# Optimization experiments

Measured on AMD Instinct MI355X. Metric: run time of the kernel, lower is better.

The kernel has to match this reference:

```python
import jax, jax.numpy as jnp
import numpy as np
from jax import lax

B, DIM, H, W = 32, 256, 64, 64
DS = DIM // 4          # dim_split = 64
MLP_H = int(DIM * 2.0)  # mlp_ratio = 2.0
AK = 11                 # att_kernel
EPS = 1e-5


def conv(x, w, b=None, padding=(0, 0), dilation=1, groups=1, stride=1):
    y = lax.conv_general_dilated(
        x, w, (stride, stride),
        [(padding[0], padding[0]), (padding[1], padding[1])],
        rhs_dilation=(dilation, dilation),
        dimension_numbers=('NCHW', 'OIHW', 'NCHW'),
        feature_group_count=groups)
    if b is not None:
        y = y + b[None, :, None, None]
    return y


def bn(x):
    # BatchNorm2d, training-mode batch stats, affine at default init (gamma=1, beta=0)
    m = x.mean(axis=(0, 2, 3), keepdims=True)
    v = ((x - m) ** 2).mean(axis=(0, 2, 3), keepdims=True)
    return (x - m) * lax.rsqrt(v + EPS)


def maxpool2x2(x):
    b, c, h, w = x.shape
    xw = x.reshape(b, c, h // 2, 2, w // 2, 2).transpose(0, 1, 2, 4, 3, 5).reshape(b, c, h // 2, w // 2, 4)
    return xw.max(axis=-1), jnp.argmax(xw, axis=-1)


def maxunpool2x2(y, idx):
    b, c, h, w = y.shape
    oh = jax.nn.one_hot(idx, 4, dtype=y.dtype)  # scatter back into 2x2 window argmax slot
    out = (y[..., None] * oh).reshape(b, c, h, w, 2, 2).transpose(0, 1, 2, 4, 3, 5)
    return out.reshape(b, c, 2 * h, 2 * w)


def maxpool3(x):
    return lax.reduce_window(x, -jnp.inf, lax.max, (1, 1, 3, 3), (1, 1, 1, 1),
                             [(0, 0), (0, 0), (1, 1), (1, 1)])


def blurpool(x):
    # antialiased_cnns.BlurPool(C, stride=3): filt_size=4, reflect pad (1,2)
    f = jnp.array([1., 3., 3., 1.], dtype=x.dtype)
    k = f[:, None] * f[None, :]
    k = k / k.sum()
    c = x.shape[1]
    wgt = jnp.broadcast_to(k[None, None], (c, 1, 4, 4))
    xp = jnp.pad(x, ((0, 0), (0, 0), (1, 2), (1, 2)), mode='reflect')
    return lax.conv_general_dilated(xp, wgt, (3, 3), [(0, 0), (0, 0)],
                                    dimension_numbers=('NCHW', 'OIHW', 'NCHW'),
                                    feature_group_count=c)


def h_tf(x):
    b, c, hh, ww = x.shape
    x = jnp.pad(x, ((0, 0), (0, 0), (0, 0), (0, ww)))
    x = x.reshape(b, c, -1)[..., :-ww]
    return x.reshape(b, c, hh, 2 * ww - 1)


def inv_h_tf(x):
    b, c, hh, _ = x.shape
    x = x.reshape(b, c, -1)
    x = jnp.pad(x, ((0, 0), (0, 0), (0, hh)))
    return x.reshape(b, c, hh, 2 * hh)[..., :hh]


def v_tf(x):
    return h_tf(x.transpose(0, 1, 3, 2)).transpose(0, 1, 3, 2)


def inv_v_tf(x):
    return inv_h_tf(x.transpose(0, 1, 3, 2)).transpose(0, 1, 3, 2)


def ga12(x, p1w, p1b, c0w, c0b, spw, spb, c1w, c1b, c2w, c2b, cw, cb, sqw, sqb, p2w, p2b):
    xp, idx = maxpool2x2(x)
    c = xp.shape[1]
    h = jax.nn.relu(conv(xp, p1w, p1b))
    a1 = conv(h, c0w, c0b, padding=(2, 2), groups=c)                 # depthwise 5x5
    a2 = conv(a1, spw, spb, padding=(9, 9), dilation=3, groups=c)    # depthwise 7x7 dil3
    a1s = conv(a1, c1w, c1b)
    a2s = conv(a2, c2w, c2b)
    comb = jnp.concatenate([a1s, a2s], axis=1)
    agg = jnp.concatenate([comb.mean(axis=1, keepdims=True),
                           comb.max(axis=1, keepdims=True)], axis=1)
    sig = jax.nn.sigmoid(conv(agg, sqw, sqb, padding=(3, 3)))
    attn = conv(a1s * sig[:, 0:1] + a2s * sig[:, 1:2], cw, cb)
    h = conv(h * attn, p2w, p2b)
    return maxunpool2x2(h, idx)


def setup_inputs() -> dict:
    key = jax.random.key(0)
    ks = jax.random.split(key, 32)
    r = lambda i, shape: jax.random.normal(ks[i], shape, jnp.float32) * 0.05
    return {
        'x': jax.random.normal(ks[0], (B, DIM, H, W), jnp.float32),
        'pa_w1': r(1, (4 * DS, DS, 1, 1)),
        'pa_w2': r(2, (DS, 4 * DS, 1, 1)),
        'la_w': r(3, (DS, DS, 3, 3)),
        'mra_h1': r(4, (DS, 1, AK, 3)),
        'mra_v1': r(5, (DS, 1, 3, AK)),
        'mra_h2': r(6, (DS, 1, AK, 3)),
        'mra_v2': r(7, (DS, 1, 3, AK)),
        'g_proj1_w': r(8, (DS, DS, 1, 1)), 'g_proj1_b': r(9, (DS,)),
        'g_conv0_w': r(10, (DS, 1, 5, 5)), 'g_conv0_b': r(11, (DS,)),
        'g_sp_w': r(12, (DS, 1, 7, 7)), 'g_sp_b': r(13, (DS,)),
        'g_c1_w': r(14, (DS // 2, DS, 1, 1)), 'g_c1_b': r(15, (DS // 2,)),
        'g_c2_w': r(16, (DS // 2, DS, 1, 1)), 'g_c2_b': r(17, (DS // 2,)),
        'g_c_w': r(18, (DS, DS // 2, 1, 1)), 'g_c_b': r(19, (DS,)),
        'g_sq_w': r(20, (2, 2, 7, 7)), 'g_sq_b': r(21, (2,)),
        'g_proj2_w': r(22, (DS, DS, 1, 1)), 'g_proj2_b': r(23, (DS,)),
        'mlp_w1': r(24, (MLP_H, DIM, 1, 1)),
        'mlp_w2': r(25, (DIM, MLP_H, 1, 1)),
    }


def reference(x, pa_w1, pa_w2, la_w, mra_h1, mra_v1, mra_h2, mra_v2,
              g_proj1_w, g_proj1_b, g_conv0_w, g_conv0_b, g_sp_w, g_sp_b,
              g_c1_w, g_c1_b, g_c2_w, g_c2_b, g_c_w, g_c_b,
              g_sq_w, g_sq_b, g_proj2_w, g_proj2_b, mlp_w1, mlp_w2):
    x1, x2, x3, x4 = jnp.split(x, 4, axis=1)
    # PA: pixel attention (1x1 expand -> BN -> ReLU -> 1x1) sigmoid gate
    xa1 = x1 * jax.nn.sigmoid(conv(jax.nn.relu(bn(conv(x1, pa_w1))), pa_w2))
    # LA: 3x3 conv -> BN -> ReLU
    xa2 = jax.nn.relu(bn(conv(x2, la_w, padding=(1, 1))))
    # MRA: maxpool3x3 -> blurpool(stride3) -> 4 strip depthwise convs (+diag shear) -> BN -> sigmoid -> nearest upsample gate
    xm = blurpool(maxpool3(x3))
    ph, pv = (AK // 2, 1), (1, AK // 2)
    xh1 = conv(xm, mra_h1, padding=ph, groups=DS)
    xw1 = conv(xm, mra_v1, padding=pv, groups=DS)
    xh2 = inv_h_tf(conv(h_tf(xm), mra_h2, padding=ph, groups=DS))
    xw2 = inv_v_tf(conv(v_tf(xm), mra_v2, padding=pv, groups=DS))
    gate = jax.nn.sigmoid(bn(xh1 + xw1 + xh2 + xw2))
    hs, ws = gate.shape[-2:]
    ri = (jnp.arange(H) * hs) // H   # torch F.interpolate mode='nearest' index rule
    ci = (jnp.arange(W) * ws) // W
    xa3 = x3 * gate[:, :, ri][:, :, :, ci]
    # D_GA (stage==2): maxpool -> GA12 -> BN -> maxunpool
    x4p, idx1 = maxpool2x2(x4)
    xg = ga12(x4p, g_proj1_w, g_proj1_b, g_conv0_w, g_conv0_b, g_sp_w, g_sp_b,
              g_c1_w, g_c1_b, g_c2_w, g_c2_b, g_c_w, g_c_b, g_sq_w, g_sq_b,
              g_proj2_w, g_proj2_b)
    xa4 = maxunpool2x2(bn(xg), idx1)
    x_att = jnp.concatenate([xa1, xa2, xa3, xa4], axis=1)
    # residual MLP (drop_path=0 -> identity)
    return x + conv(jax.nn.relu(bn(conv(x_att, mlp_w1))), mlp_w2)
```

## Files before the change

### kernel.cpp

```cpp
#include <hip/hip_runtime.h>
#include <hip/hip_bf16.h>
#include <math.h>

typedef __hip_bfloat16 bf16;
typedef __attribute__((ext_vector_type(4))) float f32x4;
typedef __attribute__((ext_vector_type(8))) short s16x8;
typedef __attribute__((ext_vector_type(4))) short s16x4;

static __device__ __forceinline__ float bits2f(short s){ return __uint_as_float(((unsigned)(unsigned short)s)<<16); }
static __device__ __forceinline__ short bfbits(float f){ bf16 h = __float2bfloat16(f); return *reinterpret_cast<short*>(&h); }
static __device__ __forceinline__ float ldf(float v){ return v; }
static __device__ __forceinline__ float sigm(float v){ return 1.f/(1.f+__expf(-v)); }

#define P_IMG 4096

#define GLDS16(SRC, DST) __builtin_amdgcn_global_load_lds( \
    (__attribute__((address_space(1))) void*)(SRC), \
    (__attribute__((address_space(3))) void*)(DST), 16, 0, 0)

namespace {
constexpr long long XATT_OFF = 0;
constexpr long long BIG_OFF  = 67108864;
constexpr long long MISC     = 134217728;
constexpr long long XM_OFF   = MISC;
constexpr long long MSUM_OFF = MISC + 3964928;
constexpr long long SH_OFF   = MISC + 7929856;
constexpr long long SH2_OFF  = MISC + 15679488;
constexpr long long X4P_OFF  = MISC + 23429120;
constexpr long long IDX1_OFF = MISC + 31817728;
constexpr long long XP_OFF   = MISC + 40206336;
constexpr long long IDX2_OFF = MISC + 42303488;
constexpr long long HBUF_OFF = MISC + 44400640;
constexpr long long A1_OFF   = MISC + 46497792;
constexpr long long A2_OFF   = MISC + 48594944;
constexpr long long A1S_OFF  = MISC + 50692096;
constexpr long long A2S_OFF  = MISC + 51740672;
constexpr long long AGG_OFF  = MISC + 52789248;
constexpr long long SIG_OFF  = MISC + 52854784;
constexpr long long ATTN_OFF = MISC + 52920320;
constexpr long long H2_OFF   = MISC + 55017472;
constexpr long long XG_OFF   = MISC + 57114624;
constexpr long long P33_OFF  = 201326592;
constexpr long long STATS_OFF= 234881024;
constexpr long long WS_NEED  = 234897408;
constexpr long long XPM_OFF  = MISC;
constexpr long long YLA_OFF  = MISC + 33554432;
}

__global__ __launch_bounds__(256) void zero_out_k(float* __restrict__ o, int n){
    int i = blockIdx.x*256 + threadIdx.x;
    if (i < n) o[i] = 0.f;
}

__global__ __launch_bounds__(256) void packw_k(const float* __restrict__ W, short* __restrict__ Wp,
                                               int kshift, int OT16)
{
    int i = blockIdx.x*256 + threadIdx.x;
    int o = i >> kshift;
    int k = i & ((1<<kshift)-1);
    long dest = (((((long)(k>>6)*2 + ((k>>5)&1))*OT16 + (o>>4))*4 + ((k>>3)&3))*16 + (o&15))*8 + (k&7);
    Wp[dest] = bfbits(W[i]);
}

__global__ __launch_bounds__(256) void packw_la_k(const float* __restrict__ W, short* __restrict__ Wp)
{
    int i = blockIdx.x*256 + threadIdx.x;
    int o = i / 576, k = i - o*576;
    int tap = k >> 6, c = k & 63;
    long dest = (((((long)(k>>6)*2 + ((k>>5)&1))*4 + (o>>4))*4 + ((k>>3)&3))*16 + (o&15))*8 + (k&7);
    Wp[dest] = bfbits(W[(o*64 + c)*9 + tap]);
}

__global__ __launch_bounds__(256) void xpose_pm_k(const float* __restrict__ x, short* __restrict__ xpm)
{
    int i = blockIdx.x*256 + threadIdx.x;
    int px = i & 4095, og = (i >> 12) & 15, b = i >> 16;
    s16x8 ov;
    #pragma unroll
    for (int j=0;j<8;j++)
        ov[j] = bfbits(x[((long)b*256 + og*8 + j)*P_IMG + px]);
    *(s16x8*)&xpm[((long)b*P_IMG + px)*128 + og*8] = ov;
}

template<int MT>
__global__ __launch_bounds__(256) void convmfma_dma_k(
    const short* __restrict__ in, int inCtot, int inOff,
    const short* __restrict__ Wp, int K, int OT16,
    short* __restrict__ out, int outC)
{
    __shared__ __align__(16) short sB[64*64];
    const int tid = threadIdx.x;
    const int b = blockIdx.z;
    const int Mbase = blockIdx.y * (32*MT);
    const int pxBase = blockIdx.x * 64;
    const int lane = tid & 63, w = tid >> 6;
    const int n16 = lane & 15, q = lane >> 4;
    const int wm = w >> 1, wn = w & 1;
    const int otBase = (Mbase>>4) + wm*MT;

    f32x4 zero = {0.f,0.f,0.f,0.f};
    f32x4 acc[MT][2];
    #pragma unroll
    for (int mt=0;mt<MT;mt++){ acc[mt][0]=zero; acc[mt][1]=zero; }

    const int drow_lo = lane >> 3;
    const int chunk = lane & 7;

    for (int kb = 0; kb < K; kb += 64){
        __syncthreads();
        #pragma unroll
        for (int s = 0; s < 2; s++){
            int seg = w*2 + s;
            int row = seg*8 + drow_lo;
            int kg = chunk ^ (row & 7);
            const short* src = in + ((long)b*P_IMG + pxBase + row)*inCtot + inOff + kb + kg*8;
            GLDS16(src, (char*)sB + seg*1024);
        }
        __syncthreads();
        #pragma unroll
        for (int kk = 0; kk < 2; kk++){
            s16x8 afr[MT], bfr[2];
            #pragma unroll
            for (int mt=0; mt<MT; mt++)
                afr[mt] = *(const s16x8*)(Wp + ((((long)(kb>>6)*2 + kk)*OT16 + otBase + mt)*64 + lane)*8);
            #pragma unroll
            for (int nt=0; nt<2; nt++){
                int n = wn*32 + nt*16 + n16;
                int g = (kk*4 + q) ^ (n & 7);
                bfr[nt] = *(const s16x8*)&sB[n*64 + (g<<3)];
            }
            #pragma unroll
            for (int mt=0; mt<MT; mt++)
                #pragma unroll
                for (int nt=0; nt<2; nt++)
                    acc[mt][nt] = __builtin_amdgcn_mfma_f32_16x16x32_bf16(afr[mt], bfr[nt], acc[mt][nt], 0, 0, 0);
        }
    }

    #pragma unroll
    for (int mt=0; mt<MT; mt++){
        #pragma unroll
        for (int nt=0; nt<2; nt++){
            int px = pxBase + wn*32 + nt*16 + n16;
            int o0 = Mbase + wm*(MT*16) + mt*16 + q*4;
            s16x4 ov;
            #pragma unroll
            for (int r=0; r<4; r++) ov[r] = bfbits(acc[mt][nt][r]);
            *(s16x4*)&out[((long)b*P_IMG + px)*outC + o0] = ov;
        }
    }
}

__global__ __launch_bounds__(256) void la_mfma_k(
    const short* __restrict__ xpm,
    const short* __restrict__ Wp,
    short* __restrict__ y)
{
    __shared__ __align__(16) short sB[64*64];
    const int tid = threadIdx.x;
    const int b = blockIdx.z;
    const int hRow = blockIdx.x;
    const int pxBase = hRow*64;
    const int lane = tid & 63, w = tid >> 6;
    const int n16 = lane & 15, q = lane >> 4;
    const int wm = w >> 1, wn = w & 1;
    const int otBase = wm*2;

    f32x4 zero = {0.f,0.f,0.f,0.f};
    f32x4 acc[2][2];
    acc[0][0]=zero; acc[0][1]=zero; acc[1][0]=zero; acc[1][1]=zero;

    const int srow = tid >> 3, schunk = tid & 7;

    for (int tap = 0; tap < 9; tap++){
        const int hh = hRow + (tap/3) - 1;
        const int dw = (tap%3) - 1;
        const bool hok = (unsigned)hh < 64u;
        s16x8 stg[2];
        #pragma unroll
        for (int it = 0; it < 2; it++){
            int row = it*32 + srow;
            int ww = row + dw;
            int kg = schunk ^ (row & 7);
            s16x8 v = {0,0,0,0,0,0,0,0};
            if (hok && (unsigned)ww < 64u)
                v = *(const s16x8*)(xpm + ((long)b*P_IMG + hh*64 + ww)*128 + 64 + kg*8);
            stg[it] = v;
        }
        __syncthreads();
        *(s16x8*)&sB[srow*64 + schunk*8]      = stg[0];
        *(s16x8*)&sB[(32+srow)*64 + schunk*8] = stg[1];
        __syncthreads();
        #pragma unroll
        for (int kk = 0; kk < 2; kk++){
            s16x8 afr[2], bfr[2];
            #pragma unroll
            for (int mt=0; mt<2; mt++)
                afr[mt] = *(const s16x8*)(Wp + ((((long)tap*2 + kk)*4 + otBase + mt)*64 + lane)*8);
            #pragma unroll
            for (int nt=0; nt<2; nt++){
                int n = wn*32 + nt*16 + n16;
                int g = (kk*4 + q) ^ (n & 7);
                bfr[nt] = *(const s16x8*)&sB[n*64 + (g<<3)];
            }
            #pragma unroll
            for (int mt=0; mt<2; mt++)
                #pragma unroll
                for (int nt=0; nt<2; nt++)
                    acc[mt][nt] = __builtin_amdgcn_mfma_f32_16x16x32_bf16(afr[mt], bfr[nt], acc[mt][nt], 0, 0, 0);
        }
    }

    #pragma unroll
    for (int mt=0; mt<2; mt++){
        #pragma unroll
        for (int nt=0; nt<2; nt++){
            int px = pxBase + wn*32 + nt*16 + n16;
            int o0 = wm*32 + mt*16 + q*4;
            s16x4 ov;
            #pragma unroll
            for (int r=0; r<4; r++) ov[r] = bfbits(acc[mt][nt][r]);
            *(s16x4*)&y[((long)b*P_IMG + px)*64 + o0] = ov;
        }
    }
}

template<int EPI, typename TOUT, int MT>
__global__ __launch_bounds__(256) void convmfma_reg_k(
    const short* __restrict__ in, int inCtot, int inOff,
    const float2* __restrict__ stats,
    const short* __restrict__ Wp, int K, int OT16,
    TOUT* __restrict__ out, int outC, int outOff,
    const float* __restrict__ aux, int auxC, int auxOff)
{
    __shared__ __align__(16) short sB[64*64];
    const int tid = threadIdx.x;
    const int b = blockIdx.z;
    const int Mbase = blockIdx.y * (32*MT);
    const int pxBase = blockIdx.x * 64;
    const int lane = tid & 63, w = tid >> 6;
    const int n16 = lane & 15, q = lane >> 4;
    const int wm = w >> 1, wn = w & 1;
    const int otBase = (Mbase>>4) + wm*MT;

    f32x4 zero = {0.f,0.f,0.f,0.f};
    f32x4 acc[MT][2];
    #pragma unroll
    for (int mt=0;mt<MT;mt++){ acc[mt][0]=zero; acc[mt][1]=zero; }

    const int srow = tid >> 3, schunk = tid & 7;
    const int skg = schunk ^ (srow & 7);

    for (int kb = 0; kb < K; kb += 64){
        const f32x4* sp = (const f32x4*)(stats + kb + skg*8);
        f32x4 p0 = sp[0], p1 = sp[1], p2 = sp[2], p3 = sp[3];
        float mm[8] = {p0[0],p0[2],p1[0],p1[2],p2[0],p2[2],p3[0],p3[2]};
        float iv[8] = {p0[1],p0[3],p1[1],p1[3],p2[1],p2[3],p3[1],p3[3]};
        s16x8 stg[2];
        #pragma unroll
        for (int it = 0; it < 2; it++){
            int row = it*32 + srow;
            s16x8 rv = *(const s16x8*)(in + ((long)b*P_IMG + pxBase + row)*inCtot + inOff + kb + skg*8);
            s16x8 ov;
            #pragma unroll
            for (int j=0;j<8;j++){
                float f = bits2f(rv[j]);
                f = (f - mm[j])*iv[j];
                f = fmaxf(f, 0.f);
                ov[j] = bfbits(f);
            }
            stg[it] = ov;
        }
        __syncthreads();
        *(s16x8*)&sB[srow*64 + schunk*8]      = stg[0];
        *(s16x8*)&sB[(32+srow)*64 + schunk*8] = stg[1];
        __syncthreads();
        #pragma unroll
        for (int kk = 0; kk < 2; kk++){
            s16x8 afr[MT], bfr[2];
            #pragma unroll
            for (int mt=0; mt<MT; mt++)
                afr[mt] = *(const s16x8*)(Wp + ((((long)(kb>>6)*2 + kk)*OT16 + otBase + mt)*64 + lane)*8);
            #pragma unroll
            for (int nt=0; nt<2; nt++){
                int n = wn*32 + nt*16 + n16;
                int g = (kk*4 + q) ^ (n & 7);
                bfr[nt] = *(const s16x8*)&sB[n*64 + (g<<3)];
            }
            #pragma unroll
            for (int mt=0; mt<MT; mt++)
                #pragma unroll
                for (int nt=0; nt<2; nt++)
                    acc[mt][nt] = __builtin_amdgcn_mfma_f32_16x16x32_bf16(afr[mt], bfr[nt], acc[mt][nt], 0, 0, 0);
        }
    }

    #pragma unroll
    for (int mt=0; mt<MT; mt++){
        #pragma unroll
        for (int nt=0; nt<2; nt++){
            int px = pxBase + wn*32 + nt*16 + n16;
            int o0 = Mbase + wm*(MT*16) + mt*16 + q*4;
            if constexpr (EPI == 1){
                s16x4 ov;
                #pragma unroll
                for (int r=0; r<4; r++){
                    float av = aux[((long)b*auxC + auxOff + o0 + r)*P_IMG + px];
                    ov[r] = bfbits(av * sigm(acc[mt][nt][r]));
                }
                *(s16x4*)&(((short*)out)[((long)b*P_IMG + px)*outC + outOff + o0]) = ov;
            } else {
                #pragma unroll
                for (int r=0; r<4; r++){
                    int o = o0 + r;
                    float av = aux[((long)b*auxC + auxOff + o)*P_IMG + px];
                    out[((long)b*outC + outOff + o)*P_IMG + px] = av + acc[mt][nt][r];
                }
            }
        }
    }
}

template<int C>
__global__ __launch_bounds__(256) void bnstats_pm_k(const short* __restrict__ in, float* __restrict__ sums)
{
    constexpr int CH8 = C/8;
    constexpr int PL  = 256/CH8;
    __shared__ float accs[2*C];
    const int t = threadIdx.x;
    for (int i=t;i<2*C;i+=256) accs[i]=0.f;
    __syncthreads();
    const int chunk = t & (CH8-1), pl = t / CH8;
    const int b = blockIdx.y;
    float s[8], s2[8];
    #pragma unroll
    for (int j=0;j<8;j++){ s[j]=0.f; s2[j]=0.f; }
    for (int px = blockIdx.x*256 + pl; px < (blockIdx.x+1)*256; px += PL){
        s16x8 v = *(const s16x8*)&in[((long)b*P_IMG + px)*C + chunk*8];
        #pragma unroll
        for (int j=0;j<8;j++){
            float f = bits2f(v[j]);
            s[j] += f; s2[j] = fmaf(f,f,s2[j]);
        }
    }
    #pragma unroll
    for (int j=0;j<8;j++){
        atomicAdd(&accs[(chunk*8+j)*2],   s[j]);
        atomicAdd(&accs[(chunk*8+j)*2+1], s2[j]);
    }
    __syncthreads();
    for (int i=t;i<2*C;i+=256) atomicAdd(&sums[i], accs[i]);
}

template<typename T>
__global__ __launch_bounds__(256) void bnstats_k(const T* __restrict__ in, int Ctot, int cOff, int Pn,
                                                 float* __restrict__ sums)
{
    const int c = blockIdx.x;
    float s=0.f, s2=0.f;
    for (int b=0;b<32;b++){
        const T* qp = in + ((long)b*Ctot + cOff + c)*Pn;
        for (int p = blockIdx.y*256 + threadIdx.x; p < Pn; p += gridDim.y*256){
            float v = ldf(qp[p]);
            s += v; s2 = fmaf(v,v,s2);
        }
    }
    __shared__ float r1[256], r2[256];
    r1[threadIdx.x]=s; r2[threadIdx.x]=s2;
    __syncthreads();
    for (int k=128;k>0;k>>=1){
        if (threadIdx.x<k){ r1[threadIdx.x]+=r1[threadIdx.x+k]; r2[threadIdx.x]+=r2[threadIdx.x+k]; }
        __syncthreads();
    }
    if (threadIdx.x==0){ atomicAdd(&sums[2*c], r1[0]); atomicAdd(&sums[2*c+1], r2[0]); }
}

__global__ __launch_bounds__(256) void bnfin_k(const float* __restrict__ sums, float2* __restrict__ minv,
                                               int C, float invN)
{
    int c = blockIdx.x*256 + threadIdx.x;
    if (c < C){
        float m = sums[2*c]*invN;
        float var = sums[2*c+1]*invN - m*m;
        minv[c] = make_float2(m, 1.f/sqrtf(var + 1e-5f));
    }
}

__global__ __launch_bounds__(256) void la_post_pm_k(const short* __restrict__ y, const float2* __restrict__ minv,
                                                    short* __restrict__ xatt)
{
    int i = blockIdx.x*256 + threadIdx.x;
    int px = i & 4095, og = (i >> 12) & 7, b = i >> 15;
    s16x8 yv = *(const s16x8*)&y[((long)b*P_IMG + px)*64 + og*8];
    s16x8 ov;
    #pragma unroll
    for (int j=0;j<8;j++){
        float2 st = minv[og*8 + j];
        float v = (bits2f(yv[j]) - st.x)*st.y;
        ov[j] = bfbits(fmaxf(v, 0.f));
    }
    *(s16x8*)&xatt[((long)b*P_IMG + px)*256 + 64 + og*8] = ov;
}

__global__ __launch_bounds__(256) void mp3_k(const float* __restrict__ x, float* __restrict__ mp){
    int i = blockIdx.x*256 + threadIdx.x;
    int b = i >> 18, c = (i >> 12) & 63, p = i & 4095;
    int h = p >> 6, wc = p & 63;
    const float* xb = x + ((long)b*256 + 128 + c)*P_IMG;
    float m = -3.4e38f;
    #pragma unroll
    for (int dh=-1; dh<=1; dh++){
        int hh = h+dh; if ((unsigned)hh>=64u) continue;
        #pragma unroll
        for (int dw=-1; dw<=1; dw++){
            int ww = wc+dw; if ((unsigned)ww>=64u) continue;
            m = fmaxf(m, xb[hh*64+ww]);
        }
    }
    mp[i] = m;
}

__global__ __launch_bounds__(256) void blur_k(const float* __restrict__ mp, float* __restrict__ xm){
    int idx = blockIdx.x*256 + threadIdx.x;
    int oj = idx % 22; int t = idx / 22; int oi = t % 22; int bc = t / 22;
    const float* mb = mp + (long)bc * P_IMG;
    const float fw[4] = {1.f,3.f,3.f,1.f};
    float s = 0.f;
    #pragma unroll
    for (int u=0;u<4;u++){
        int r = 3*oi - 1 + u;
        r = r < 0 ? -r : (r > 63 ? 126 - r : r);
        float rs = 0.f;
        #pragma unroll
        for (int v=0; v<4; v++){
            int qq = 3*oj - 1 + v;
            qq = qq < 0 ? -qq : (qq > 63 ? 126 - qq : qq);
            rs = fmaf(fw[v], mb[r*64+qq], rs);
        }
        s = fmaf(fw[u], rs, s);
    }
    xm[idx] = s * (1.f/64.f);
}

__global__ __launch_bounds__(256) void mra_conv_k(const float* __restrict__ xm,
                                                  const float* __restrict__ wh1, const float* __restrict__ wv1,
                                                  const float* __restrict__ wh2, const float* __restrict__ wv2,
                                                  float* __restrict__ msum)
{
    int idx = blockIdx.x*256 + threadIdx.x;
    int j = idx % 22; int t = idx / 22; int i = t % 22; int bc = t / 22; int c = bc & 63;
    const float* xb = xm + (long)bc*484;
    float s = 0.f;
    #pragma unroll
    for (int u=0;u<11;u++){
        int ii = i + u - 5; if ((unsigned)ii >= 22u) continue;
        #pragma unroll
        for (int v=0;v<3;v++){
            int jj = j + v - 1; if ((unsigned)jj >= 22u) continue;
            s = fmaf(wh1[c*33 + u*3 + v], xb[ii*22+jj], s);
        }
    }
    #pragma unroll
    for (int u=0;u<3;u++){
        int ii = i + u - 1; if ((unsigned)ii >= 22u) continue;
        #pragma unroll
        for (int v=0;v<11;v++){
            int jj = j + v - 5; if ((unsigned)jj >= 22u) continue;
            s = fmaf(wv1[c*33 + u*11 + v], xb[ii*22+jj], s);
        }
    }
    {
        int f = i*44 + j; int r = f/43; int q = f - 43*r;
        #pragma unroll
        for (int u=0;u<11;u++){
            int a = r + u - 5; if ((unsigned)a >= 22u) continue;
            #pragma unroll
            for (int v=0;v<3;v++){
                int bcol = q + v - 1; if ((unsigned)bcol >= 43u) continue;
                int g = a*43 + bcol; int rr = g/44; int qq = g - 44*rr;
                if (qq < 22) s = fmaf(wh2[c*33 + u*3 + v], xb[rr*22+qq], s);
            }
        }
    }
    {
        int g = j*44 + i; int r = g/43; int q = g - 43*r;
        #pragma unroll
        for (int u=0;u<3;u++){
            int a = q + u - 1; if ((unsigned)a >= 43u) continue;
            #pragma unroll
            for (int v=0;v<11;v++){
                int bcol = r + v - 5; if ((unsigned)bcol >= 22u) continue;
                int g2 = bcol*43 + a; int rr = g2/44; int qq = g2 - 44*rr;
                if (qq < 22) s = fmaf(wv2[c*33 + u*11 + v], xb[qq*22+rr], s);
            }
        }
    }
    msum[idx] = s;
}

__global__ __launch_bounds__(256) void mra_gate_pm_k(const float* __restrict__ x, const float* __restrict__ msum,
                                                     const float2* __restrict__ minv, short* __restrict__ xatt)
{
    int i = blockIdx.x*256 + threadIdx.x;
    int px = i & 4095, og = (i >> 12) & 7, b = i >> 15;
    int h = px >> 6, wcol = px & 63;
    int ri = (h*22) >> 6, ci = (wcol*22) >> 6;
    s16x8 ov;
    #pragma unroll
    for (int j=0;j<8;j++){
        int c = og*8 + j;
        float g = msum[((long)b*64 + c)*484 + ri*22 + ci];
        float2 st = minv[c];
        g = sigm((g - st.x)*st.y);
        float xv = x[((long)b*256 + 128 + c)*P_IMG + px];
        ov[j] = bfbits(xv * g);
    }
    *(s16x8*)&xatt[((long)b*P_IMG + px)*256 + 128 + og*8] = ov;
}

__global__ __launch_bounds__(256) void pool1_k(const float* __restrict__ x, float* __restrict__ x4p,
                                               int* __restrict__ idx1)
{
    int i = blockIdx.x*256 + threadIdx.x;
    int b = i >> 16, c = (i >> 10) & 63, s = i & 1023;
    int y = s >> 5, xc = s & 31;
    const float* xb = x + ((long)b*256 + 192 + c)*P_IMG;
    float v00 = xb[(2*y)*64 + 2*xc];
    float v01 = xb[(2*y)*64 + 2*xc + 1];
    float v10 = xb[(2*y+1)*64 + 2*xc];
    float v11 = xb[(2*y+1)*64 + 2*xc + 1];
    float best = v00; int bi = 0;
    if (v01 > best){ best = v01; bi = 1; }
    if (v10 > best){ best = v10; bi = 2; }
    if (v11 > best){ best = v11; bi = 3; }
    x4p[i] = best; idx1[i] = bi;
}

__global__ __launch_bounds__(256) void pool2_k(const float* __restrict__ x4p, float* __restrict__ xp,
                                               int* __restrict__ idx2)
{
    int i = blockIdx.x*256 + threadIdx.x;
    int b = i >> 14, c = (i >> 8) & 63, s = i & 255;
    int y = s >> 4, xc = s & 15;
    const float* xb = x4p + ((long)b*64 + c)*1024;
    float v00 = xb[(2*y)*32 + 2*xc];
    float v01 = xb[(2*y)*32 + 2*xc + 1];
    float v10 = xb[(2*y+1)*32 + 2*xc];
    float v11 = xb[(2*y+1)*32 + 2*xc + 1];
    float best = v00; int bi = 0;
    if (v01 > best){ best = v01; bi = 1; }
    if (v10 > best){ best = v10; bi = 2; }
    if (v11 > best){ best = v11; bi = 3; }
    xp[i] = best; idx2[i] = bi;
}

__global__ __launch_bounds__(256) void ga_proj_k(const float* __restrict__ in, const float* __restrict__ mul,
                                                 const float* __restrict__ w, const float* __restrict__ bias,
                                                 float* __restrict__ out, int Cout, int relu)
{
    int s = threadIdx.x, og = blockIdx.x, b = blockIdx.y;
    float acc[8];
    #pragma unroll
    for (int j=0;j<8;j++) acc[j]=0.f;
    for (int c=0;c<64;c++){
        float v = in[((long)b*64 + c)*256 + s];
        if (mul) v *= mul[((long)b*64 + c)*256 + s];
        #pragma unroll
        for (int j=0;j<8;j++) acc[j] = fmaf(v, w[(og*8 + j)*64 + c], acc[j]);
    }
    #pragma unroll
    for (int j=0;j<8;j++){
        int o = og*8 + j;
        float val = acc[j] + bias[o];
        if (relu) val = fmaxf(val, 0.f);
        out[((long)b*Cout + o)*256 + s] = val;
    }
}

__global__ __launch_bounds__(256) void ga_dw5_k(const float* __restrict__ h, const float* __restrict__ w,
                                                const float* __restrict__ bias, float* __restrict__ a1)
{
    int i = blockIdx.x*256 + threadIdx.x;
    int b = i >> 14, c = (i >> 8) & 63, s = i & 255;
    int y = s >> 4, x = s & 15;
    const float* hb = h + ((long)b*64 + c)*256;
    float acc = bias[c];
    #pragma unroll
    for (int u=0;u<5;u++){
        int yy = y + u - 2; if ((unsigned)yy >= 16u) continue;
        #pragma unroll
        for (int v=0;v<5;v++){
            int xx = x + v - 2; if ((unsigned)xx >= 16u) continue;
            acc = fmaf(w[c*25 + u*5 + v], hb[yy*16 + xx], acc);
        }
    }
    a1[i] = acc;
}

__global__ __launch_bounds__(256) void ga_dw7_k(const float* __restrict__ a1, const float* __restrict__ w,
                                                const float* __restrict__ bias, float* __restrict__ a2)
{
    int i = blockIdx.x*256 + threadIdx.x;
    int b = i >> 14, c = (i >> 8) & 63, s = i & 255;
    int y = s >> 4, x = s & 15;
    const float* ab = a1 + ((long)b*64 + c)*256;
    float acc = bias[c];
    #pragma unroll
    for (int u=0;u<7;u++){
        int yy = y + 3*(u-3); if ((unsigned)yy >= 16u) continue;
        #pragma unroll
        for (int v=0;v<7;v++){
            int xx = x + 3*(v-3); if ((unsigned)xx >= 16u) continue;
            acc = fmaf(w[c*49 + u*7 + v], ab[yy*16 + xx], acc);
        }
    }
    a2[i] = acc;
}

__global__ __launch_bounds__(256) void ga_agg_k(const float* __restrict__ a1s, const float* __restrict__ a2s,
                                                float* __restrict__ agg)
{
    int i = blockIdx.x*256 + threadIdx.x;
    int b = i >> 8, s = i & 255;
    float sum = 0.f, mx = -3.4e38f;
    for (int c=0;c<32;c++){
        float v = a1s[((long)b*32 + c)*256 + s];
        sum += v; mx = fmaxf(mx, v);
    }
    for (int c=0;c<32;c++){
        float v = a2s[((long)b*32 + c)*256 + s];
        sum += v; mx = fmaxf(mx, v);
    }
    agg[((long)b*2 + 0)*256 + s] = sum * (1.f/64.f);
    agg[((long)b*2 + 1)*256 + s] = mx;
}

__global__ __launch_bounds__(256) void ga_sq_k(const float* __restrict__ agg, const float* __restrict__ w,
                                               const float* __restrict__ bias, float* __restrict__ sig)
{
    int i = blockIdx.x*256 + threadIdx.x;
    int b = i >> 9, o = (i >> 8) & 1, s = i & 255;
    int y = s >> 4, x = s & 15;
    float acc = bias[o];
    for (int ic=0; ic<2; ic++){
        const float* ab = agg + ((long)b*2 + ic)*256;
        #pragma unroll
        for (int u=0;u<7;u++){
            int yy = y + u - 3; if ((unsigned)yy >= 16u) continue;
            #pragma unroll
            for (int v=0;v<7;v++){
                int xx = x + v - 3; if ((unsigned)xx >= 16u) continue;
                acc = fmaf(w[((o*2 + ic)*7 + u)*7 + v], ab[yy*16 + xx], acc);
            }
        }
    }
    sig[i] = sigm(acc);
}

__global__ __launch_bounds__(256) void ga_attn_k(const float* __restrict__ a1s, const float* __restrict__ a2s,
                                                 const float* __restrict__ sig, const float* __restrict__ w,
                                                 const float* __restrict__ bias, float* __restrict__ attn)
{
    int s = threadIdx.x, og = blockIdx.x, b = blockIdx.y;
    float s0 = sig[((long)b*2 + 0)*256 + s];
    float s1 = sig[((long)b*2 + 1)*256 + s];
    float acc[8];
    #pragma unroll
    for (int j=0;j<8;j++) acc[j]=0.f;
    for (int c=0;c<32;c++){
        float v = a1s[((long)b*32 + c)*256 + s]*s0 + a2s[((long)b*32 + c)*256 + s]*s1;
        #pragma unroll
        for (int j=0;j<8;j++) acc[j] = fmaf(v, w[(og*8 + j)*32 + c], acc[j]);
    }
    #pragma unroll
    for (int j=0;j<8;j++){
        int o = og*8 + j;
        attn[((long)b*64 + o)*256 + s] = acc[j] + bias[o];
    }
}

__global__ __launch_bounds__(256) void ga_unpool1_k(const float* __restrict__ h2, const int* __restrict__ idx2,
                                                    float* __restrict__ xg)
{
    int i = blockIdx.x*256 + threadIdx.x;
    int b = i >> 16, c = (i >> 10) & 63, s = i & 1023;
    int Y = s >> 5, X = s & 31;
    int slot = ((Y & 1) << 1) | (X & 1);
    long pi = ((long)b*64 + c)*256 + (Y >> 1)*16 + (X >> 1);
    xg[i] = (idx2[pi] == slot) ? h2[pi] : 0.f;
}

__global__ __launch_bounds__(256) void ga_out_pm_k(const float* __restrict__ xg, const int* __restrict__ idx1,
                                                   const float2* __restrict__ minv, short* __restrict__ xatt)
{
    int i = blockIdx.x*256 + threadIdx.x;
    int px = i & 4095, og = (i >> 12) & 7, b = i >> 15;
    int hh = px >> 6, ww = px & 63;
    int slot = ((hh & 1) << 1) | (ww & 1);
    s16x8 ov;
    #pragma unroll
    for (int j=0;j<8;j++){
        int c = og*8 + j;
        long pi = ((long)b*64 + c)*1024 + (hh >> 1)*32 + (ww >> 1);
        float v = 0.f;
        if (idx1[pi] == slot){
            float2 st = minv[c];
            v = (xg[pi] - st.x)*st.y;
        }
        ov[j] = bfbits(v);
    }
    *(s16x8*)&xatt[((long)b*P_IMG + px)*256 + 192 + og*8] = ov;
}

extern "C" void kernel_launch(void* const* d_in, const int* in_sizes, int n_in,
                              void* d_out, int out_size, void* d_ws, size_t ws_size,
                              hipStream_t stream)
{
    const float* x      = (const float*)d_in[0];
    const float* pa_w1  = (const float*)d_in[1];
    const float* pa_w2  = (const float*)d_in[2];
    const float* la_w   = (const float*)d_in[3];
    const float* mra_h1 = (const float*)d_in[4];
    const float* mra_v1 = (const float*)d_in[5];
    const float* mra_h2 = (const float*)d_in[6];
    const float* mra_v2 = (const float*)d_in[7];
    const float* g_p1w  = (const float*)d_in[8];
    const float* g_p1b  = (const float*)d_in[9];
    const float* g_c0w  = (const float*)d_in[10];
    const float* g_c0b  = (const float*)d_in[11];
    const float* g_spw  = (const float*)d_in[12];
    const float* g_spb  = (const float*)d_in[13];
    const float* g_c1w  = (const float*)d_in[14];
    const float* g_c1b  = (const float*)d_in[15];
    const float* g_c2w  = (const float*)d_in[16];
    const float* g_c2b  = (const float*)d_in[17];
    const float* g_cw   = (const float*)d_in[18];
    const float* g_cb   = (const float*)d_in[19];
    const float* g_sqw  = (const float*)d_in[20];
    const float* g_sqb  = (const float*)d_in[21];
    const float* g_p2w  = (const float*)d_in[22];
    const float* g_p2b  = (const float*)d_in[23];
    const float* mlp_w1 = (const float*)d_in[24];
    const float* mlp_w2 = (const float*)d_in[25];
    float* outp = (float*)d_out;
    char* ws = (char*)d_ws;

    if (ws_size < (size_t)WS_NEED){
        zero_out_k<<<(out_size + 255)/256, 256, 0, stream>>>(outp, out_size);
        return;
    }

    short* xatt = (short*)(ws + XATT_OFF);
    short* tbuf = (short*)(ws + BIG_OFF);
    short* xpm  = (short*)(ws + XPM_OFF);
    short* yla  = (short*)(ws + YLA_OFF);
    float* xm   = (float*)(ws + XM_OFF);
    float* msum = (float*)(ws + MSUM_OFF);
    float* x4p  = (float*)(ws + X4P_OFF);
    int*   idx1 = (int*)(ws + IDX1_OFF);
    float* xp   = (float*)(ws + XP_OFF);
    int*   idx2 = (int*)(ws + IDX2_OFF);
    float* hbuf = (float*)(ws + HBUF_OFF);
    float* a1   = (float*)(ws + A1_OFF);
    float* a2   = (float*)(ws + A2_OFF);
    float* a1s  = (float*)(ws + A1S_OFF);
    float* a2s  = (float*)(ws + A2S_OFF);
    float* agg  = (float*)(ws + AGG_OFF);
    float* sig  = (float*)(ws + SIG_OFF);
    float* attn = (float*)(ws + ATTN_OFF);
    float* h2   = (float*)(ws + H2_OFF);
    float* xg   = (float*)(ws + XG_OFF);
    float* p33  = (float*)(ws + P33_OFF);
    float* raw  = (float*)(ws + STATS_OFF);
    float*  raw_pa  = raw;
    float*  raw_la  = raw + 512;
    float*  raw_mra = raw + 640;
    float*  raw_ga  = raw + 768;
    float*  raw_mlp = raw + 896;
    float2* mv_pa   = (float2*)(raw + 1920);
    float2* mv_la   = mv_pa + 256;
    float2* mv_mra  = mv_la + 64;
    float2* mv_ga   = mv_mra + 64;
    float2* mv_mlp  = mv_ga + 64;

    hipMemsetAsync(raw, 0, 1920*sizeof(float), stream);

    short* wp_pa1 = (short*)(ws + P33_OFF);
    short* wp_pa2 = wp_pa1 + 256*64;
    short* wp_la  = wp_pa2 + 64*256;
    packw_k<<<64,256,0,stream>>>(pa_w1, wp_pa1, 6, 16);
    packw_k<<<64,256,0,stream>>>(pa_w2, wp_pa2, 8, 4);
    packw_la_k<<<144,256,0,stream>>>(la_w, wp_la);

    xpose_pm_k<<<8192,256,0,stream>>>(x, xpm);

    convmfma_dma_k<4><<<dim3(64,2,32),256,0,stream>>>(xpm,128,0, wp_pa1,64,16, tbuf,256);
    bnstats_pm_k<256><<<dim3(16,32),256,0,stream>>>(tbuf, raw_pa);
    bnfin_k<<<1,256,0,stream>>>(raw_pa, mv_pa, 256, 1.f/131072.f);
    convmfma_reg_k<1,short,2><<<dim3(64,1,32),256,0,stream>>>(tbuf,256,0, mv_pa, wp_pa2,256,4,
                                                              xatt,256,0, x,256,0);

    la_mfma_k<<<dim3(64,1,32),256,0,stream>>>(xpm, wp_la, yla);
    bnstats_pm_k<64><<<dim3(16,32),256,0,stream>>>(yla, raw_la);
    bnfin_k<<<1,256,0,stream>>>(raw_la, mv_la, 64, 1.f/131072.f);
    la_post_pm_k<<<4096,256,0,stream>>>(yla, mv_la, xatt);

    mp3_k<<<32768,256,0,stream>>>(x, p33);
    blur_k<<<3872,256,0,stream>>>(p33, xm);
    mra_conv_k<<<3872,256,0,stream>>>(xm, mra_h1, mra_v1, mra_h2, mra_v2, msum);
    bnstats_k<float><<<dim3(64,2),256,0,stream>>>(msum,64,0,484, raw_mra);
    bnfin_k<<<1,256,0,stream>>>(raw_mra, mv_mra, 64, 1.f/15488.f);
    mra_gate_pm_k<<<4096,256,0,stream>>>(x, msum, mv_mra, xatt);

    pool1_k<<<8192,256,0,stream>>>(x, x4p, idx1);
    pool2_k<<<2048,256,0,stream>>>(x4p, xp, idx2);
    ga_proj_k<<<dim3(8,32),256,0,stream>>>(xp, nullptr, g_p1w, g_p1b, hbuf, 64, 1);
    ga_dw5_k<<<2048,256,0,stream>>>(hbuf, g_c0w, g_c0b, a1);
    ga_dw7_k<<<2048,256,0,stream>>>(a1, g_spw, g_spb, a2);
    ga_proj_k<<<dim3(4,32),256,0,stream>>>(a1, nullptr, g_c1w, g_c1b, a1s, 32, 0);
    ga_proj_k<<<dim3(4,32),256,0,stream>>>(a2, nullptr, g_c2w, g_c2b, a2s, 32, 0);
    ga_agg_k<<<32,256,0,stream>>>(a1s, a2s, agg);
    ga_sq_k<<<64,256,0,stream>>>(agg, g_sqw, g_sqb, sig);
    ga_attn_k<<<dim3(8,32),256,0,stream>>>(a1s, a2s, sig, g_cw, g_cb, attn);
    ga_proj_k<<<dim3(8,32),256,0,stream>>>(hbuf, attn, g_p2w, g_p2b, h2, 64, 0);
    ga_unpool1_k<<<8192,256,0,stream>>>(h2, idx2, xg);
    bnstats_k<float><<<dim3(64,4),256,0,stream>>>(xg,64,0,1024, raw_ga);
    bnfin_k<<<1,256,0,stream>>>(raw_ga, mv_ga, 64, 1.f/32768.f);
    ga_out_pm_k<<<4096,256,0,stream>>>(xg, idx1, mv_ga, xatt);

    short* wm1 = (short*)(ws + P33_OFF);
    short* wm2 = wm1 + 512*256;
    packw_k<<<512,256,0,stream>>>(mlp_w1, wm1, 8, 32);
    packw_k<<<512,256,0,stream>>>(mlp_w2, wm2, 9, 16);
    convmfma_dma_k<4><<<dim3(64,4,32),256,0,stream>>>(xatt,256,0, wm1,256,32, tbuf,512);
    bnstats_pm_k<512><<<dim3(16,32),256,0,stream>>>(tbuf, raw_mlp);
    bnfin_k<<<2,256,0,stream>>>(raw_mlp, mv_mlp, 512, 1.f/131072.f);
    convmfma_reg_k<2,float,4><<<dim3(64,2,32),256,0,stream>>>(tbuf,512,0, mv_mlp, wm2,512,16,
                                                              outp,256,0, x,256,0);
}
```

Measured before the change: 980.7 us.

## Double-buffer LDS tiles and prefetch next K-slice in MFMA conv kernels

Three MFMA conv kernels (DMA 1x1, 3x3 local attention, and the BN-ReLU register-staged one) switch to double-buffered LDS. Each iteration now issues the global loads for the next K tile or tap while the current one is being multiplied, and replaces the pair of __syncthreads with explicit waitcnt and barrier instructions. The aim is to hide global memory latency behind MFMA work. In exchange it doubles LDS use, which may lower occupancy, and relies on hand-counted vmcnt values that are only valid for MT==4. Two unused workspace offset constants are also removed.

Result: faster. 960.8 us (-2.0%).

```diff
diff --git a/kernel.cpp b/kernel.cpp
--- a/kernel.cpp
+++ b/kernel.cpp
@@ -24,8 +24,6 @@
 constexpr long long MISC     = 134217728;
 constexpr long long XM_OFF   = MISC;
 constexpr long long MSUM_OFF = MISC + 3964928;
-constexpr long long SH_OFF   = MISC + 7929856;
-constexpr long long SH2_OFF  = MISC + 15679488;
 constexpr long long X4P_OFF  = MISC + 23429120;
 constexpr long long IDX1_OFF = MISC + 31817728;
 constexpr long long XP_OFF   = MISC + 40206336;
@@ -88,7 +86,8 @@
     const short* __restrict__ Wp, int K, int OT16,
     short* __restrict__ out, int outC)
 {
-    __shared__ __align__(16) short sB[64*64];
+    static_assert(MT == 4, "vmcnt counts assume MT==4");
+    __shared__ __align__(16) short sB[2][64*64];
     const int tid = threadIdx.x;
     const int b = blockIdx.z;
     const int Mbase = blockIdx.y * (32*MT);
@@ -105,36 +104,56 @@
 
     const int drow_lo = lane >> 3;
     const int chunk = lane & 7;
-
-    for (int kb = 0; kb < K; kb += 64){
-        __syncthreads();
-        #pragma unroll
-        for (int s = 0; s < 2; s++){
-            int seg = w*2 + s;
-            int row = seg*8 + drow_lo;
-            int kg = chunk ^ (row & 7);
-            const short* src = in + ((long)b*P_IMG + pxBase + row)*inCtot + inOff + kb + kg*8;
-            GLDS16(src, (char*)sB + seg*1024);
-        }
-        __syncthreads();
+    const int seg0 = w*2, seg1 = w*2 + 1;
+    const int row0 = seg0*8 + drow_lo, row1 = seg1*8 + drow_lo;
+    const int kg0 = chunk ^ (row0 & 7), kg1 = chunk ^ (row1 & 7);
+    const short* src0 = in + ((long)b*P_IMG + pxBase + row0)*inCtot + inOff + kg0*8;
+    const short* src1 = in + ((long)b*P_IMG + pxBase + row1)*inCtot + inOff + kg1*8;
+
+    const int NT = K >> 6;
+    GLDS16(src0, (char*)&sB[0][0] + seg0*1024);
+    GLDS16(src1, (char*)&sB[0][0] + seg1*1024);
+
+    for (int t = 0; t < NT; t++){
+        const int kb = t << 6;
+        s16x8 afr[2][MT];
+        #pragma unroll
+        for (int kk=0; kk<2; kk++)
+            #pragma unroll
+            for (int mt=0; mt<MT; mt++)
+                afr[kk][mt] = *(const s16x8*)(Wp + ((((long)t*2 + kk)*OT16 + otBase + mt)*64 + lane)*8);
+        __builtin_amdgcn_sched_barrier(0);
+        if (t+1 < NT){
+            GLDS16(src0 + kb + 64, (char*)&sB[(t+1)&1][0] + seg0*1024);
+            GLDS16(src1 + kb + 64, (char*)&sB[(t+1)&1][0] + seg1*1024);
+            __builtin_amdgcn_sched_barrier(0);
+            asm volatile("s_waitcnt vmcnt(10)" ::: "memory");
+        } else {
+            __builtin_amdgcn_sched_barrier(0);
+            asm volatile("s_waitcnt vmcnt(8)" ::: "memory");
+        }
+        __builtin_amdgcn_sched_barrier(0);
+        __builtin_amdgcn_s_barrier();
+        __builtin_amdgcn_sched_barrier(0);
+        const short* sC = &sB[t&1][0];
         #pragma unroll
         for (int kk = 0; kk < 2; kk++){
-            s16x8 afr[MT], bfr[2];
-            #pragma unroll
-            for (int mt=0; mt<MT; mt++)
-                afr[mt] = *(const s16x8*)(Wp + ((((long)(kb>>6)*2 + kk)*OT16 + otBase + mt)*64 + lane)*8);
+            s16x8 bfr[2];
             #pragma unroll
             for (int nt=0; nt<2; nt++){
                 int n = wn*32 + nt*16 + n16;
                 int g = (kk*4 + q) ^ (n & 7);
-                bfr[nt] = *(const s16x8*)&sB[n*64 + (g<<3)];
+                bfr[nt] = *(const s16x8*)&sC[n*64 + (g<<3)];
             }
             #pragma unroll
             for (int mt=0; mt<MT; mt++)
                 #pragma unroll
                 for (int nt=0; nt<2; nt++)
-                    acc[mt][nt] = __builtin_amdgcn_mfma_f32_16x16x32_bf16(afr[mt], bfr[nt], acc[mt][nt], 0, 0, 0);
-        }
+                    acc[mt][nt] = __builtin_amdgcn_mfma_f32_16x16x32_bf16(afr[kk][mt], bfr[nt], acc[mt][nt], 0, 0, 0);
+        }
+        __builtin_amdgcn_sched_barrier(0);
+        __builtin_amdgcn_s_barrier();
+        __builtin_amdgcn_sched_barrier(0);
     }
 
     #pragma unroll
@@ -156,7 +175,7 @@
     const short* __restrict__ Wp,
     short* __restrict__ y)
 {
-    __shared__ __align__(16) short sB[64*64];
+    __shared__ __align__(16) short sB[2][64*64];
     const int tid = threadIdx.x;
     const int b = blockIdx.z;
     const int hRow = blockIdx.x;
@@ -171,26 +190,34 @@
     acc[0][0]=zero; acc[0][1]=zero; acc[1][0]=zero; acc[1][1]=zero;
 
     const int srow = tid >> 3, schunk = tid & 7;
+    const int kgA = schunk ^ (srow & 7);
+
+    auto tapload = [&](int tap, s16x8& v0, s16x8& v1){
+        int hh = hRow + (tap/3) - 1;
+        int dw = (tap%3) - 1;
+        bool hok = (unsigned)hh < 64u;
+        s16x8 z = {0,0,0,0,0,0,0,0};
+        v0 = z; v1 = z;
+        int w0 = srow + dw, w1 = 32 + srow + dw;
+        if (hok && (unsigned)w0 < 64u)
+            v0 = *(const s16x8*)(xpm + ((long)b*P_IMG + hh*64 + w0)*128 + 64 + kgA*8);
+        if (hok && (unsigned)w1 < 64u)
+            v1 = *(const s16x8*)(xpm + ((long)b*P_IMG + hh*64 + w1)*128 + 64 + kgA*8);
+    };
+
+    s16x8 cv0, cv1;
+    tapload(0, cv0, cv1);
 
     for (int tap = 0; tap < 9; tap++){
-        const int hh = hRow + (tap/3) - 1;
-        const int dw = (tap%3) - 1;
-        const bool hok = (unsigned)hh < 64u;
-        s16x8 stg[2];
-        #pragma unroll
-        for (int it = 0; it < 2; it++){
-            int row = it*32 + srow;
-            int ww = row + dw;
-            int kg = schunk ^ (row & 7);
-            s16x8 v = {0,0,0,0,0,0,0,0};
-            if (hok && (unsigned)ww < 64u)
-                v = *(const s16x8*)(xpm + ((long)b*P_IMG + hh*64 + ww)*128 + 64 + kg*8);
-            stg[it] = v;
-        }
-        __syncthreads();
-        *(s16x8*)&sB[srow*64 + schunk*8]      = stg[0];
-        *(s16x8*)&sB[(32+srow)*64 + schunk*8] = stg[1];
-        __syncthreads();
+        s16x8 nv0 = cv0, nv1 = cv1;
+        if (tap+1 < 9) tapload(tap+1, nv0, nv1);
+        *(s16x8*)&sB[tap&1][srow*64 + schunk*8]      = cv0;
+        *(s16x8*)&sB[tap&1][(32+srow)*64 + schunk*8] = cv1;
+        asm volatile("s_waitcnt lgkmcnt(0)" ::: "memory");
+        __builtin_amdgcn_sched_barrier(0);
+        __builtin_amdgcn_s_barrier();
+        __builtin_amdgcn_sched_barrier(0);
+        const short* sC = &sB[tap&1][0];
         #pragma unroll
         for (int kk = 0; kk < 2; kk++){
             s16x8 afr[2], bfr[2];
@@ -201,7 +228,7 @@
             for (int nt=0; nt<2; nt++){
                 int n = wn*32 + nt*16 + n16;
                 int g = (kk*4 + q) ^ (n & 7);
-                bfr[nt] = *(const s16x8*)&sB[n*64 + (g<<3)];
+                bfr[nt] = *(const s16x8*)&sC[n*64 + (g<<3)];
             }
             #pragma unroll
             for (int mt=0; mt<2; mt++)
@@ -209,6 +236,10 @@
                 for (int nt=0; nt<2; nt++)
                     acc[mt][nt] = __builtin_amdgcn_mfma_f32_16x16x32_bf16(afr[mt], bfr[nt], acc[mt][nt], 0, 0, 0);
         }
+        __builtin_amdgcn_sched_barrier(0);
+        __builtin_amdgcn_s_barrier();
+        __builtin_amdgcn_sched_barrier(0);
+        cv0 = nv0; cv1 = nv1;
     }
 
     #pragma unroll
@@ -233,7 +264,7 @@
     TOUT* __restrict__ out, int outC, int outOff,
     const float* __restrict__ aux, int auxC, int auxOff)
 {
-    __shared__ __align__(16) short sB[64*64];
+    __shared__ __align__(16) short sB[2][64*64];
     const int tid = threadIdx.x;
     const int b = blockIdx.z;
     const int Mbase = blockIdx.y * (32*MT);
@@ -250,42 +281,59 @@
 
     const int srow = tid >> 3, schunk = tid & 7;
     const int skg = schunk ^ (srow & 7);
-
-    for (int kb = 0; kb < K; kb += 64){
-        const f32x4* sp = (const f32x4*)(stats + kb + skg*8);
-        f32x4 p0 = sp[0], p1 = sp[1], p2 = sp[2], p3 = sp[3];
+    const short* inrow0 = in + ((long)b*P_IMG + pxBase + srow)*inCtot + inOff + skg*8;
+    const short* inrow1 = in + ((long)b*P_IMG + pxBase + 32 + srow)*inCtot + inOff + skg*8;
+    const float2* stp = stats + skg*8;
+
+    const int NT = K >> 6;
+    s16x8 rv0 = *(const s16x8*)(inrow0);
+    s16x8 rv1 = *(const s16x8*)(inrow1);
+    const f32x4* sp0 = (const f32x4*)(stp);
+    f32x4 p0 = sp0[0], p1 = sp0[1], p2 = sp0[2], p3 = sp0[3];
+
+    for (int t = 0; t < NT; t++){
+        const int kb = t << 6;
+        s16x8 nrv0 = rv0, nrv1 = rv1;
+        f32x4 q0 = p0, q1 = p1, q2 = p2, q3 = p3;
+        if (t+1 < NT){
+            nrv0 = *(const s16x8*)(inrow0 + kb + 64);
+            nrv1 = *(const s16x8*)(inrow1 + kb + 64);
+            const f32x4* np = (const f32x4*)(stp + kb + 64);
+            q0 = np[0]; q1 = np[1]; q2 = np[2]; q3 = np[3];
+        }
         float mm[8] = {p0[0],p0[2],p1[0],p1[2],p2[0],p2[2],p3[0],p3[2]};
         float iv[8] = {p0[1],p0[3],p1[1],p1[3],p2[1],p2[3],p3[1],p3[3]};
-        s16x8 stg[2];
-        #pragma unroll
-        for (int it = 0; it < 2; it++){
-            int row = it*32 + srow;
-            s16x8 rv = *(const s16x8*)(in + ((long)b*P_IMG + pxBase + row)*inCtot + inOff + kb + skg*8);
-            s16x8 ov;
-            #pragma unroll
-            for (int j=0;j<8;j++){
-                float f = bits2f(rv[j]);
-                f = (f - mm[j])*iv[j];
-                f = fmaxf(f, 0.f);
-                ov[j] = bfbits(f);
-            }
-            stg[it] = ov;
-        }
-        __syncthreads();
-        *(s16x8*)&sB[srow*64 + schunk*8]      = stg[0];
-        *(s16x8*)&sB[(32+srow)*64 + schunk*8] = stg[1];
-        __syncthreads();
+        s16x8 sg0, sg1;
+        #pragma unroll
+        for (int j=0;j<8;j++){
+            float f = bits2f(rv0[j]);
+            f = (f - mm[j])*iv[j];
+            sg0[j] = bfbits(fmaxf(f, 0.f));
+        }
+        #pragma unroll
+        for (int j=0;j<8;j++){
+            float f = bits2f(rv1[j]);
+            f = (f - mm[j])*iv[j];
+            sg1[j] = bfbits(fmaxf(f, 0.f));
+        }
+        *(s16x8*)&sB[t&1][srow*64 + schunk*8]      = sg0;
+        *(s16x8*)&sB[t&1][(32+srow)*64 + schunk*8] = sg1;
+        asm volatile("s_waitcnt lgkmcnt(0)" ::: "memory");
+        __builtin_amdgcn_sched_barrier(0);
+        __builtin_amdgcn_s_barrier();
+        __builtin_amdgcn_sched_barrier(0);
+        const short* sC = &sB[t&1][0];
         #pragma unroll
         for (int kk = 0; kk < 2; kk++){
             s16x8 afr[MT], bfr[2];
             #pragma unroll
             for (int mt=0; mt<MT; mt++)
-                afr[mt] = *(const s16x8*)(Wp + ((((long)(kb>>6)*2 + kk)*OT16 + otBase + mt)*64 + lane)*8);
+                afr[mt] = *(const s16x8*)(Wp + ((((long)t*2 + kk)*OT16 + otBase + mt)*64 + lane)*8);
             #pragma unroll
             for (int nt=0; nt<2; nt++){
                 int n = wn*32 + nt*16 + n16;
                 int g = (kk*4 + q) ^ (n & 7);
-                bfr[nt] = *(const s16x8*)&sB[n*64 + (g<<3)];
+                bfr[nt] = *(const s16x8*)&sC[n*64 + (g<<3)];
             }
             #pragma unroll
             for (int mt=0; mt<MT; mt++)
@@ -293,6 +341,11 @@
                 for (int nt=0; nt<2; nt++)
                     acc[mt][nt] = __builtin_amdgcn_mfma_f32_16x16x32_bf16(afr[mt], bfr[nt], acc[mt][nt], 0, 0, 0);
         }
+        __builtin_amdgcn_sched_barrier(0);
+        __builtin_amdgcn_s_barrier();
+        __builtin_amdgcn_sched_barrier(0);
+        rv0 = nrv0; rv1 = nrv1;
+        p0 = q0; p1 = q1; p2 = q2; p3 = q3;
     }
 
     #pragma unroll
```
